# Kernel optimization log

Measured on AMD Instinct MI355X. Metric: run time of the kernel, lower is better.

The kernel has to match this reference:

```python
import jax, jax.numpy as jnp
import numpy as np
import math

# dims
C2, C1, T = 32, 64, 2048      # x shape
AVGF = 32                     # num_submatrices
SEG = T // AVGF               # 64
M = C1 * C2                   # M_size1 = 2048
TK = 3                        # num_blocks
HA = 16                       # num_heads
DH = M // HA                  # 128
EPS = 1e-5


def setup_inputs() -> dict:
    key = jax.random.key(0)
    ks = jax.random.split(key, 12)
    sc = 0.02  # scale params to keep fp32 activations finite
    return {
        "x": jax.random.normal(ks[0], (C2, C1, T), dtype=jnp.float32),
        "weight": jax.random.normal(ks[1], (M, M), dtype=jnp.float32) * sc,
        "Wqkv": jax.random.normal(ks[2], (TK, 3, HA, DH, M), dtype=jnp.float32) * sc,
        "Wo": jax.random.normal(ks[3], (TK, M, M), dtype=jnp.float32) * sc,
        "ln1_g": jnp.ones((M,), jnp.float32),
        "ln1_b": jnp.zeros((M,), jnp.float32),
        "ln2_g": jnp.ones((M,), jnp.float32),
        "ln2_b": jnp.zeros((M,), jnp.float32),
        "fc1_w": jax.random.normal(ks[4], (4 * M, M), dtype=jnp.float32) * sc,
        "fc1_b": jnp.zeros((4 * M,), jnp.float32),
        "fc2_w": jax.random.normal(ks[5], (M, 4 * M), dtype=jnp.float32) * sc,
        "fc2_b": jnp.zeros((M,), jnp.float32),
    }


def _ln(x, g, b):
    mu = jnp.mean(x, axis=-1, keepdims=True)
    var = jnp.var(x, axis=-1, keepdims=True)
    return (x - mu) / jnp.sqrt(var + EPS) * g + b


def _sinusoidal_bias():
    # bias[i, 2j]   = sin(i / 10000**(2*(2j)/M))  -- exponent uses even column index
    # bias[i, 2j+1] = cos(same angle)
    i = jnp.arange(AVGF, dtype=jnp.float32)[:, None]          # [avgf, 1]
    j = jnp.arange(0, M, 2, dtype=jnp.float32)[None, :]       # [1, M/2] even cols
    ang = i / jnp.power(10000.0, 2.0 * j / M)                 # [avgf, M/2]
    return jnp.stack([jnp.sin(ang), jnp.cos(ang)], axis=-1).reshape(AVGF, M)


def reference(x, weight, Wqkv, Wo, ln1_g, ln1_b, ln2_g, ln2_b,
              fc1_w, fc1_b, fc2_w, fc2_b):
    inp = jnp.transpose(x, (2, 1, 0))                          # [T, C1, C2]
    # segment-average over time -> [avgf, C1, C2]
    inputc = inp.reshape(AVGF, SEG, C1, C2).mean(axis=1)
    altx = inputc.reshape(AVGF, M)                             # [avgf, M]
    s = jnp.einsum('lm,im->il', weight, altx)                  # [avgf, M]
    s = s + _sinusoidal_bias()
    inv_sqrt_dh = 1.0 / math.sqrt(DH)
    for a in range(TK):                                        # fixed small block loop
        y = _ln(s, ln1_g, ln1_b)
        qkv = jnp.einsum('xhdm,im->xihd', Wqkv[a], y)          # [3, avgf, hA, Dh]
        q, k, v = qkv[0], qkv[1], qkv[2]
        rsa = jnp.einsum('ihd,ihd->ih', q * inv_sqrt_dh, k)    # per-token scalar attn
        imv = jnp.cumsum(rsa[..., None] * v, axis=0)           # serial inter-block scan
        s = jnp.einsum('nm,im->in', Wo[a], imv.reshape(AVGF, M)) + s
        s = _ln(s, ln2_g, ln2_b) + s
        h = jax.nn.gelu(s @ fc1_w.T + fc1_b, approximate=False)
        s = h @ fc2_w.T + fc2_b
    return s.reshape(AVGF, C1, C2)
```

## Files before the change

kernel.cpp:

```cpp
#include <hip/hip_runtime.h>
#include <math.h>

typedef __attribute__((ext_vector_type(4))) float f32x4;
typedef __attribute__((ext_vector_type(8))) short bf16x8;

__device__ inline short f2bf(float f) {
    union { float f; unsigned u; } v; v.f = f;
    unsigned u = v.u;
    u += 0x7fffu + ((u >> 16) & 1u);
    return (short)(u >> 16);
}

__global__ __launch_bounds__(256) void k_avg_init(const float* __restrict__ x,
                                                  float* __restrict__ altx,
                                                  float* __restrict__ s) {
    int blk = blockIdx.x, t = threadIdx.x;
    if (blk < 512) {
        int wv = t >> 6, lane = t & 63;
        int p = blk * 4 + wv;
        const float* row = x + (size_t)p * 2048;
        int c2 = p >> 6, c1 = p & 63;
        int m = c1 * 32 + c2;
        for (int seg = 0; seg < 32; ++seg) {
            float v = row[seg * 64 + lane];
            for (int off = 32; off; off >>= 1) v += __shfl_xor(v, off, 64);
            if (lane == 0) altx[seg * 2048 + m] = v * (1.0f / 64.0f);
        }
    } else {
        int i = blk - 512;
        const float kln = logf(10000.0f) / 1024.0f;
        for (int l = t; l < 2048; l += 256) {
            int c = l & ~1;
            float ang = (float)i * expf(-(float)c * kln);
            s[i * 2048 + l] = (l & 1) ? cosf(ang) : sinf(ang);
        }
    }
}

__device__ inline void row_stats(const float* __restrict__ row, float& mu, float& rstd) {
    float sm = 0.f, ss = 0.f;
    for (int idx = threadIdx.x; idx < 2048; idx += 256) {
        float v = row[idx]; sm += v; ss += v * v;
    }
    for (int off = 32; off; off >>= 1) {
        sm += __shfl_xor(sm, off, 64);
        ss += __shfl_xor(ss, off, 64);
    }
    __shared__ float as[4], bs[4];
    int wv = threadIdx.x >> 6, lane = threadIdx.x & 63;
    if (lane == 0) { as[wv] = sm; bs[wv] = ss; }
    __syncthreads();
    sm = as[0] + as[1] + as[2] + as[3];
    ss = bs[0] + bs[1] + bs[2] + bs[3];
    mu = sm * (1.0f / 2048.0f);
    float var = ss * (1.0f / 2048.0f) - mu * mu;
    rstd = rsqrtf(var + 1e-5f);
}

__global__ __launch_bounds__(256) void k_prep1(const float* __restrict__ s,
                                               const float* __restrict__ g,
                                               const float* __restrict__ b,
                                               float* __restrict__ y,
                                               float* __restrict__ qkv) {
    int blk = blockIdx.x;
    if (blk < 32) {
        const float* row = s + blk * 2048;
        float mu, rstd; row_stats(row, mu, rstd);
        float* yr = y + blk * 2048;
        for (int idx = threadIdx.x; idx < 2048; idx += 256)
            yr[idx] = (row[idx] - mu) * rstd * g[idx] + b[idx];
    } else {
        int z = blk - 32;
        float4* p4 = (float4*)(qkv + (size_t)z * 8192);
        float4 zero = {0.f, 0.f, 0.f, 0.f};
        for (int idx = threadIdx.x; idx < 2048; idx += 256) p4[idx] = zero;
    }
}

__global__ __launch_bounds__(256) void k_scan(const float* __restrict__ qkv,
                                              const float* __restrict__ s,
                                              float* __restrict__ imv,
                                              float* __restrict__ s2) {
    int blk = blockIdx.x, t = threadIdx.x;
    if (blk < 16) {
        int h = blk;
        __shared__ float rsa[32];
        if (t < 32) {
            const float* qr = qkv + (size_t)t * 6144 + h * 128;
            const float* kr = qr + 2048;
            float acc = 0.f;
            for (int d = 0; d < 128; ++d) acc += qr[d] * kr[d];
            rsa[t] = acc * 0.08838834764831845f;
        }
        __syncthreads();
        if (t < 128) {
            float acc = 0.f;
            for (int i = 0; i < 32; ++i) {
                acc += rsa[i] * qkv[(size_t)i * 6144 + 4096 + h * 128 + t];
                imv[i * 2048 + h * 128 + t] = acc;
            }
        }
    } else {
        int z = blk - 16;
        const float4* sp = (const float4*)(s + (size_t)z * 2048);
        float4* dp = (float4*)(s2 + (size_t)z * 2048);
        for (int idx = t; idx < 512; idx += 256) dp[idx] = sp[idx];
    }
}

__global__ __launch_bounds__(256) void k_prep2(const float* __restrict__ s2,
                                               const float* __restrict__ g,
                                               const float* __restrict__ b,
                                               float* __restrict__ sout,
                                               float* __restrict__ h) {
    int blk = blockIdx.x;
    if (blk < 32) {
        const float* row = s2 + blk * 2048;
        float mu, rstd; row_stats(row, mu, rstd);
        float* sr = sout + blk * 2048;
        for (int idx = threadIdx.x; idx < 2048; idx += 256) {
            float v = row[idx];
            sr[idx] = (v - mu) * rstd * g[idx] + b[idx] + v;
        }
    } else {
        int z = blk - 32;
        float4* p4 = (float4*)(h + (size_t)z * 8192);
        float4 zero = {0.f, 0.f, 0.f, 0.f};
        for (int idx = threadIdx.x; idx < 2048; idx += 256) p4[idx] = zero;
    }
}

__global__ __launch_bounds__(256) void k_act(float* __restrict__ h,
                                             const float* __restrict__ fc1_b,
                                             float* __restrict__ sout,
                                             const float* __restrict__ fc2_b) {
    int blk = blockIdx.x, t = threadIdx.x;
    if (blk < 128) {
        size_t base = ((size_t)blk * 256 + t) * 8;
        #pragma unroll
        for (int j = 0; j < 8; ++j) {
            size_t idx = base + j;
            float v = h[idx] + fc1_b[idx & 8191];
            h[idx] = 0.5f * v * (1.0f + erff(v * 0.70710678118654752f));
        }
    } else {
        size_t base = ((size_t)(blk - 128) * 256 + t) * 8;
        #pragma unroll
        for (int j = 0; j < 8; ++j) {
            size_t idx = base + j;
            sout[idx] = fc2_b[idx & 2047];
        }
    }
}

__global__ __launch_bounds__(256) void k_gemm(const float* __restrict__ W,
                                              const float* __restrict__ act,
                                              float* __restrict__ out,
                                              int N, int K, int kchunk) {
    int t = threadIdx.x;
    int lane = t & 63, wv = t >> 6;
    int m = lane & 15, q = lane >> 4;
    int nb = blockIdx.x * 64 + wv * 16;
    size_t kbeg = (size_t)blockIdx.y * kchunk;
    const float* A0 = act + (size_t)m * K + kbeg + q * 8;
    const float* A1 = A0 + (size_t)16 * K;
    const float* B  = W + (size_t)(nb + m) * K + kbeg + q * 8;
    f32x4 acc0 = {0.f, 0.f, 0.f, 0.f};
    f32x4 acc1 = {0.f, 0.f, 0.f, 0.f};
    for (int k = 0; k < kchunk; k += 32) {
        float4 a0l = *(const float4*)(A0 + k);
        float4 a0h = *(const float4*)(A0 + k + 4);
        float4 a1l = *(const float4*)(A1 + k);
        float4 a1h = *(const float4*)(A1 + k + 4);
        float4 bl  = *(const float4*)(B + k);
        float4 bh  = *(const float4*)(B + k + 4);
        bf16x8 fa0 = { f2bf(a0l.x), f2bf(a0l.y), f2bf(a0l.z), f2bf(a0l.w),
                       f2bf(a0h.x), f2bf(a0h.y), f2bf(a0h.z), f2bf(a0h.w) };
        bf16x8 fa1 = { f2bf(a1l.x), f2bf(a1l.y), f2bf(a1l.z), f2bf(a1l.w),
                       f2bf(a1h.x), f2bf(a1h.y), f2bf(a1h.z), f2bf(a1h.w) };
        bf16x8 fb  = { f2bf(bl.x),  f2bf(bl.y),  f2bf(bl.z),  f2bf(bl.w),
                       f2bf(bh.x),  f2bf(bh.y),  f2bf(bh.z),  f2bf(bh.w) };
        acc0 = __builtin_amdgcn_mfma_f32_16x16x32_bf16(fa0, fb, acc0, 0, 0, 0);
        acc1 = __builtin_amdgcn_mfma_f32_16x16x32_bf16(fa1, fb, acc1, 0, 0, 0);
    }
    float* op = out + (size_t)(q * 4) * N + nb + m;
    #pragma unroll
    for (int r = 0; r < 4; ++r) {
        atomicAdd(op + (size_t)r * N, acc0[r]);
        atomicAdd(op + (size_t)(r + 16) * N, acc1[r]);
    }
}

extern "C" void kernel_launch(void* const* d_in, const int* in_sizes, int n_in,
                              void* d_out, int out_size, void* d_ws, size_t ws_size,
                              hipStream_t stream) {
    const float* x      = (const float*)d_in[0];
    const float* weight = (const float*)d_in[1];
    const float* Wqkv   = (const float*)d_in[2];
    const float* Wo     = (const float*)d_in[3];
    const float* ln1_g  = (const float*)d_in[4];
    const float* ln1_b  = (const float*)d_in[5];
    const float* ln2_g  = (const float*)d_in[6];
    const float* ln2_b  = (const float*)d_in[7];
    const float* fc1_w  = (const float*)d_in[8];
    const float* fc1_b  = (const float*)d_in[9];
    const float* fc2_w  = (const float*)d_in[10];
    const float* fc2_b  = (const float*)d_in[11];
    float* ws   = (float*)d_ws;
    float* altx = ws;
    float* sbuf = ws + 65536;
    float* y    = ws + 131072;
    float* s2   = ws + 196608;
    float* imv  = ws + 262144;
    float* qkv  = ws + 327680;
    float* h    = ws + 524288;
    float* outF = (float*)d_out;

    k_avg_init<<<544, 256, 0, stream>>>(x, altx, sbuf);
    k_gemm<<<dim3(32, 16), 256, 0, stream>>>(weight, altx, sbuf, 2048, 2048, 128);
    for (int a = 0; a < 3; ++a) {
        k_prep1<<<56, 256, 0, stream>>>(sbuf, ln1_g, ln1_b, y, qkv);
        k_gemm<<<dim3(96, 8), 256, 0, stream>>>(Wqkv + (size_t)a * 12582912, y, qkv, 6144, 2048, 256);
        k_scan<<<48, 256, 0, stream>>>(qkv, sbuf, imv, s2);
        k_gemm<<<dim3(32, 16), 256, 0, stream>>>(Wo + (size_t)a * 4194304, imv, s2, 2048, 2048, 128);
        k_prep2<<<64, 256, 0, stream>>>(s2, ln2_g, ln2_b, sbuf, h);
        k_gemm<<<dim3(128, 4), 256, 0, stream>>>(fc1_w, sbuf, h, 8192, 2048, 512);
        float* sout = (a == 2) ? outF : sbuf;
        k_act<<<160, 256, 0, stream>>>(h, fc1_b, sout, fc2_b);
        k_gemm<<<dim3(32, 16), 256, 0, stream>>>(fc2_w, h, sout, 2048, 8192, 512);
    }
}
```

Before: 632.1 us.

## Stage activation tile in LDS and prefetch all weight K-slices up front

```diff
diff --git a/kernel.cpp b/kernel.cpp
--- a/kernel.cpp
+++ b/kernel.cpp
@@ -153,36 +153,54 @@
     }
 }
 
-__global__ __launch_bounds__(256) void k_gemm(const float* __restrict__ W,
-                                              const float* __restrict__ act,
-                                              float* __restrict__ out,
-                                              int N, int K, int kchunk) {
+template<int KC, int TAG>
+__global__ __launch_bounds__(256, 2) void k_gemm(const float* __restrict__ W,
+                                                 const float* __restrict__ act,
+                                                 float* __restrict__ out,
+                                                 int N, int K) {
+    constexpr int S = KC / 32;
+    __shared__ short lAs[32][KC + 8];
     int t = threadIdx.x;
     int lane = t & 63, wv = t >> 6;
     int m = lane & 15, q = lane >> 4;
     int nb = blockIdx.x * 64 + wv * 16;
-    size_t kbeg = (size_t)blockIdx.y * kchunk;
-    const float* A0 = act + (size_t)m * K + kbeg + q * 8;
-    const float* A1 = A0 + (size_t)16 * K;
-    const float* B  = W + (size_t)(nb + m) * K + kbeg + q * 8;
-    f32x4 acc0 = {0.f, 0.f, 0.f, 0.f};
-    f32x4 acc1 = {0.f, 0.f, 0.f, 0.f};
-    for (int k = 0; k < kchunk; k += 32) {
-        float4 a0l = *(const float4*)(A0 + k);
-        float4 a0h = *(const float4*)(A0 + k + 4);
-        float4 a1l = *(const float4*)(A1 + k);
-        float4 a1h = *(const float4*)(A1 + k + 4);
-        float4 bl  = *(const float4*)(B + k);
-        float4 bh  = *(const float4*)(B + k + 4);
-        bf16x8 fa0 = { f2bf(a0l.x), f2bf(a0l.y), f2bf(a0l.z), f2bf(a0l.w),
-                       f2bf(a0h.x), f2bf(a0h.y), f2bf(a0h.z), f2bf(a0h.w) };
-        bf16x8 fa1 = { f2bf(a1l.x), f2bf(a1l.y), f2bf(a1l.z), f2bf(a1l.w),
-                       f2bf(a1h.x), f2bf(a1h.y), f2bf(a1h.z), f2bf(a1h.w) };
-        bf16x8 fb  = { f2bf(bl.x),  f2bf(bl.y),  f2bf(bl.z),  f2bf(bl.w),
-                       f2bf(bh.x),  f2bf(bh.y),  f2bf(bh.z),  f2bf(bh.w) };
+    size_t kbeg = (size_t)blockIdx.y * KC;
+
+    constexpr int APT = KC / 8;
+    int arow = t >> 3, acol = (t & 7) * APT;
+    const float* ap = act + (size_t)arow * K + kbeg + acol;
+    float4 areg[APT / 4];
+    #pragma unroll
+    for (int j = 0; j < APT / 4; ++j) areg[j] = *(const float4*)(ap + j * 4);
+
+    const float* B = W + (size_t)(nb + m) * K + kbeg + q * 8;
+    float4 Bb[2 * S];
+    #pragma unroll
+    for (int s = 0; s < S; ++s) {
+        Bb[2 * s]     = *(const float4*)(B + s * 32);
+        Bb[2 * s + 1] = *(const float4*)(B + s * 32 + 4);
+    }
+
+    #pragma unroll
+    for (int j = 0; j < APT / 4; ++j) {
+        short4 c = { f2bf(areg[j].x), f2bf(areg[j].y), f2bf(areg[j].z), f2bf(areg[j].w) };
+        *(short4*)&lAs[arow][acol + j * 4] = c;
+    }
+    __syncthreads();
+
+    f32x4 acc0 = {0.f,0.f,0.f,0.f};
+    f32x4 acc1 = {0.f,0.f,0.f,0.f};
+    #pragma unroll
+    for (int s = 0; s < S; ++s) {
+        bf16x8 fa0 = *(const bf16x8*)&lAs[m][s * 32 + q * 8];
+        bf16x8 fa1 = *(const bf16x8*)&lAs[m + 16][s * 32 + q * 8];
+        float4 bl = Bb[2 * s], bh = Bb[2 * s + 1];
+        bf16x8 fb = { f2bf(bl.x), f2bf(bl.y), f2bf(bl.z), f2bf(bl.w),
+                      f2bf(bh.x), f2bf(bh.y), f2bf(bh.z), f2bf(bh.w) };
         acc0 = __builtin_amdgcn_mfma_f32_16x16x32_bf16(fa0, fb, acc0, 0, 0, 0);
         acc1 = __builtin_amdgcn_mfma_f32_16x16x32_bf16(fa1, fb, acc1, 0, 0, 0);
     }
+
     float* op = out + (size_t)(q * 4) * N + nb + m;
     #pragma unroll
     for (int r = 0; r < 4; ++r) {
@@ -217,16 +235,16 @@
     float* outF = (float*)d_out;
 
     k_avg_init<<<544, 256, 0, stream>>>(x, altx, sbuf);
-    k_gemm<<<dim3(32, 16), 256, 0, stream>>>(weight, altx, sbuf, 2048, 2048, 128);
+    k_gemm<128, 0><<<dim3(32, 16), 256, 0, stream>>>(weight, altx, sbuf, 2048, 2048);
     for (int a = 0; a < 3; ++a) {
         k_prep1<<<56, 256, 0, stream>>>(sbuf, ln1_g, ln1_b, y, qkv);
-        k_gemm<<<dim3(96, 8), 256, 0, stream>>>(Wqkv + (size_t)a * 12582912, y, qkv, 6144, 2048, 256);
+        k_gemm<128, 1><<<dim3(96, 16), 256, 0, stream>>>(Wqkv + (size_t)a * 12582912, y, qkv, 6144, 2048);
         k_scan<<<48, 256, 0, stream>>>(qkv, sbuf, imv, s2);
-        k_gemm<<<dim3(32, 16), 256, 0, stream>>>(Wo + (size_t)a * 4194304, imv, s2, 2048, 2048, 128);
+        k_gemm<128, 2><<<dim3(32, 16), 256, 0, stream>>>(Wo + (size_t)a * 4194304, imv, s2, 2048, 2048);
         k_prep2<<<64, 256, 0, stream>>>(s2, ln2_g, ln2_b, sbuf, h);
-        k_gemm<<<dim3(128, 4), 256, 0, stream>>>(fc1_w, sbuf, h, 8192, 2048, 512);
+        k_gemm<128, 3><<<dim3(128, 16), 256, 0, stream>>>(fc1_w, sbuf, h, 8192, 2048);
         float* sout = (a == 2) ? outF : sbuf;
         k_act<<<160, 256, 0, stream>>>(h, fc1_b, sout, fc2_b);
-        k_gemm<<<dim3(32, 16), 256, 0, stream>>>(fc2_w, h, sout, 2048, 8192, 512);
-    }
-}
+        k_gemm<256, 4><<<dim3(32, 32), 256, 0, stream>>>(fc2_w, h, sout, 2048, 8192);
+    }
+}
```

Result: faster. 552.7 us (-12.6%).
